# Kernel tuning notes

Hardware: AMD Instinct MI355X
Metric: run time of the kernel (lower is better)

## Reference

```python
import jax, jax.numpy as jnp
import numpy as np

# Qwen3-0.6B-like config; 4 equal-length requests flattened into [R*S, H]
L, R, S, H = 2, 4, 1024, 1024
NH, NKV, DH = 16, 8, 128
FF = 3072
EPS = 1e-6
THETA = 1e6
SCALE = 0.02  # weight init scale to keep activations sane


def setup_inputs() -> dict:
    key = jax.random.key(0)
    ks = jax.random.split(key, 8)
    return {
        "hidden_states": jax.random.normal(ks[0], (R * S, H), jnp.float32),
        "Wq": jax.random.normal(ks[1], (L, H, NH * DH), jnp.float32) * SCALE,
        "Wk": jax.random.normal(ks[2], (L, H, NKV * DH), jnp.float32) * SCALE,
        "Wv": jax.random.normal(ks[3], (L, H, NKV * DH), jnp.float32) * SCALE,
        "Wo": jax.random.normal(ks[4], (L, NH * DH, H), jnp.float32) * SCALE,
        "q_norm_w": jnp.ones((L, DH), jnp.float32),
        "k_norm_w": jnp.ones((L, DH), jnp.float32),
        "ln1_w": jnp.ones((L, H), jnp.float32),
        "ln2_w": jnp.ones((L, H), jnp.float32),
        "Wg": jax.random.normal(ks[5], (L, H, FF), jnp.float32) * SCALE,
        "Wu": jax.random.normal(ks[6], (L, H, FF), jnp.float32) * SCALE,
        "Wd": jax.random.normal(ks[7], (L, FF, H), jnp.float32) * SCALE,
        "final_norm_w": jnp.ones((H,), jnp.float32),
    }


def _rms(x, w):
    return x * jax.lax.rsqrt(jnp.mean(x * x, axis=-1, keepdims=True) + EPS) * w


def _rope_tables():
    inv_freq = 1.0 / (THETA ** (jnp.arange(0, DH, 2, dtype=jnp.float32) / DH))
    pos = jnp.arange(S, dtype=jnp.float32)  # per-request positions 0..S-1 (prefill)
    freqs = pos[:, None] * inv_freq[None, :]        # [S, DH/2]
    emb = jnp.concatenate([freqs, freqs], axis=-1)  # [S, DH]
    return jnp.cos(emb), jnp.sin(emb)


def _rotate_half(x):
    x1, x2 = jnp.split(x, 2, axis=-1)
    return jnp.concatenate([-x2, x1], axis=-1)


def _apply_rope(x, cos, sin):
    # x: [R, heads, S, DH]; cos/sin: [S, DH]
    c = cos[None, None]
    s = sin[None, None]
    return x * c + _rotate_half(x) * s


def reference(hidden_states, Wq, Wk, Wv, Wo, q_norm_w, k_norm_w, ln1_w, ln2_w,
              Wg, Wu, Wd, final_norm_w):
    cos, sin = _rope_tables()
    causal = jnp.tril(jnp.ones((S, S), dtype=bool))  # per-request causal mask
    neg = jnp.finfo(hidden_states.dtype).min
    scaling = 1.0 / jnp.sqrt(jnp.asarray(DH, hidden_states.dtype))

    x = hidden_states
    for l in range(L):
        # --- attention block ---
        residual = x
        h = _rms(x, ln1_w[l])                       # [R*S, H]
        q = (h @ Wq[l]).reshape(R, S, NH, DH)
        k = (h @ Wk[l]).reshape(R, S, NKV, DH)
        v = (h @ Wv[l]).reshape(R, S, NKV, DH)
        q = _rms(q, q_norm_w[l]).transpose(0, 2, 1, 3)   # [R, NH, S, DH]
        k = _rms(k, k_norm_w[l]).transpose(0, 2, 1, 3)   # [R, NKV, S, DH]
        v = v.transpose(0, 2, 1, 3)                      # [R, NKV, S, DH]
        q = _apply_rope(q, cos, sin)
        k = _apply_rope(k, cos, sin)
        # GQA: repeat KV heads
        rep = NH // NKV
        k = jnp.repeat(k, rep, axis=1)
        v = jnp.repeat(v, rep, axis=1)
        scores = jnp.einsum('rhqd,rhkd->rhqk', q, k) * scaling
        scores = jnp.where(causal[None, None], scores, neg)
        attn = jax.nn.softmax(scores, axis=-1)
        o = jnp.einsum('rhqk,rhkd->rhqd', attn, v)       # [R, NH, S, DH]
        o = o.transpose(0, 2, 1, 3).reshape(R * S, NH * DH)
        x = residual + o @ Wo[l]
        # --- MLP block ---
        residual = x
        h = _rms(x, ln2_w[l])
        x = residual + (jax.nn.silu(h @ Wg[l]) * (h @ Wu[l])) @ Wd[l]
    return _rms(x, final_norm_w)
```

## Files before the change

kernel.cpp:

```cpp
#include <hip/hip_runtime.h>
#include <hip/hip_bf16.h>

typedef __bf16 bf16;
typedef __bf16 bf16x8 __attribute__((ext_vector_type(8)));
typedef float f32x4 __attribute__((ext_vector_type(4)));

#define DEVINL __device__ __forceinline__

constexpr int L_ = 2, R_ = 4, S_ = 1024, H_ = 1024;
constexpr int NH_ = 16, NKV_ = 8, DH_ = 128;
constexpr int FF_ = 3072;
constexpr int T_ = R_ * S_;

DEVINL void gload16(const bf16* g, bf16* l) {
    __builtin_amdgcn_global_load_lds(
        (const __attribute__((address_space(1))) void*)g,
        (__attribute__((address_space(3))) void*)l, 16, 0, 0);
}

__global__ void rope_tables_kernel(float* __restrict__ cosb, float* __restrict__ sinb) {
    int s = blockIdx.x;
    int i = threadIdx.x;
    float inv = __expf(-(float)i * (1.0f / 64.0f) * 13.815510557964274f);
    float f = (float)s * inv;
    cosb[s * 64 + i] = cosf(f);
    sinb[s * 64 + i] = sinf(f);
}

template <bool OUT_BF16>
__global__ __launch_bounds__(256) void rmsnorm_kernel(const float* __restrict__ x,
                                                      const float* __restrict__ w,
                                                      void* __restrict__ out) {
    int row = blockIdx.x;
    const float* xr = x + (size_t)row * H_;
    int t = threadIdx.x;
    f32x4 v = *(const f32x4*)(xr + t * 4);
    float ss = v[0] * v[0] + v[1] * v[1] + v[2] * v[2] + v[3] * v[3];
#pragma unroll
    for (int off = 32; off; off >>= 1) ss += __shfl_xor(ss, off);
    __shared__ float part[4];
    if ((t & 63) == 0) part[t >> 6] = ss;
    __syncthreads();
    ss = part[0] + part[1] + part[2] + part[3];
    float r = rsqrtf(ss * (1.0f / (float)H_) + 1e-6f);
    f32x4 wv = *(const f32x4*)(w + t * 4);
#pragma unroll
    for (int j = 0; j < 4; ++j) {
        float o = v[j] * r * wv[j];
        if constexpr (OUT_BF16)
            ((bf16*)out)[(size_t)row * H_ + t * 4 + j] = (bf16)o;
        else
            ((float*)out)[(size_t)row * H_ + t * 4 + j] = o;
    }
}

__global__ __launch_bounds__(256) void transpose_all_kernel(
    const float* __restrict__ Wq, const float* __restrict__ Wk, const float* __restrict__ Wv,
    const float* __restrict__ Wo, const float* __restrict__ Wg, const float* __restrict__ Wu,
    const float* __restrict__ Wd, bf16* __restrict__ wqkv_t, bf16* __restrict__ wo_t,
    bf16* __restrict__ wgu_t, bf16* __restrict__ wd_t) {
    __shared__ float tile[32][33];
    int bid = blockIdx.x;
    const float* in;
    bf16* out;
    int Rk, Cn, mode, tid;
    if (bid < 2048) { in = Wq; out = wqkv_t; Rk = 1024; Cn = 2048; mode = 0; tid = bid; }
    else if (bid < 3072) { in = Wk; out = wqkv_t + (size_t)2048 * 1024; Rk = 1024; Cn = 1024; mode = 0; tid = bid - 2048; }
    else if (bid < 4096) { in = Wv; out = wqkv_t + (size_t)3072 * 1024; Rk = 1024; Cn = 1024; mode = 0; tid = bid - 3072; }
    else if (bid < 6144) { in = Wo; out = wo_t; Rk = 2048; Cn = 1024; mode = 0; tid = bid - 4096; }
    else if (bid < 9216) { in = Wg; out = wgu_t; Rk = 1024; Cn = 3072; mode = 1; tid = bid - 6144; }
    else if (bid < 12288) { in = Wu; out = wgu_t; Rk = 1024; Cn = 3072; mode = 2; tid = bid - 9216; }
    else { in = Wd; out = wd_t; Rk = 3072; Cn = 1024; mode = 0; tid = bid - 12288; }
    int nbx = Cn >> 5;
    int c0 = (tid % nbx) * 32, r0 = (tid / nbx) * 32;
    int t = threadIdx.x;
    int tc = t & 31, tr = t >> 5;
#pragma unroll
    for (int i = 0; i < 4; ++i) {
        int r = tr + i * 8;
        tile[r][tc] = in[(size_t)(r0 + r) * Cn + c0 + tc];
    }
    __syncthreads();
#pragma unroll
    for (int i = 0; i < 4; ++i) {
        int c = c0 + tr + i * 8;
        int n = (mode == 0) ? c : (((c >> 4) << 5) + ((mode == 2) ? 16 : 0) + (c & 15));
        out[(size_t)n * Rk + r0 + tc] = (bf16)tile[tc][tr + i * 8];
    }
}

__global__ __launch_bounds__(256) void vt_kernel(const bf16* __restrict__ qkv,
                                                 bf16* __restrict__ vt) {
    __shared__ bf16 tile[32][34];
    int s0 = blockIdx.x * 32, c0 = blockIdx.y * 32, r = blockIdx.z;
    int t = threadIdx.x, tc = t & 31, tr = t >> 5;
#pragma unroll
    for (int i = 0; i < 4; ++i) {
        int s = tr + i * 8;
        tile[s][tc] = qkv[(size_t)(r * 1024 + s0 + s) * 4096 + 3072 + c0 + tc];
    }
    __syncthreads();
#pragma unroll
    for (int i = 0; i < 4; ++i) {
        int c = tr + i * 8;
        vt[((size_t)(r * 1024 + c0 + c)) * 1024 + s0 + tc] = tile[tc][c];
    }
}

template <int EPI>
__global__ __launch_bounds__(512, 2) void gemmT_kernel(const bf16* __restrict__ A,
                                                       const bf16* __restrict__ Bt,
                                                       void* __restrict__ out,
                                                       int M, int N, int K) {
    __shared__ bf16 lds[49152];
    const int NT = K >> 5;
    int nbm = M >> 8, nbn = N >> 8;
    int slice = nbn >> 3;
    int id = blockIdx.x;
    int xcd = id & 7, wi = id >> 3;
    int bm = (wi / slice) << 8;
    int bn = (xcd * slice + wi % slice) << 8;
    int t = threadIdx.x, lane = t & 63, w = t >> 6;
    int wm = w >> 2, wn = w & 3;
    int hi = lane >> 4, f = lane & 15;

    int r0 = t >> 2;
    int so = (((t & 3) ^ ((r0 >> 1) & 3)) << 3);
    const bf16* aS0 = A + (size_t)(bm + r0) * K + so;
    const bf16* aS1 = A + (size_t)(bm + 128 + r0) * K + so;
    const bf16* bS0 = Bt + (size_t)(bn + r0) * K + so;
    const bf16* bS1 = Bt + (size_t)(bn + 128 + r0) * K + so;

    f32x4 acc[8][4] = {};

    auto stage = [&](int tt, int sb) {
        gload16(aS0 + tt * 32, lds + sb * 8192 + w * 512);
        gload16(aS1 + tt * 32, lds + sb * 8192 + 4096 + w * 512);
        gload16(bS0 + tt * 32, lds + 24576 + sb * 8192 + w * 512);
        gload16(bS1 + tt * 32, lds + 24576 + sb * 8192 + 4096 + w * 512);
    };

    stage(0, 0);
    stage(1, 1);
    asm volatile("s_waitcnt vmcnt(4)" ::: "memory");
    __builtin_amdgcn_s_barrier();

    int cb = 0;
    for (int tau = 0; tau < NT; ++tau) {
        const bf16* aB = lds + cb * 8192;
        const bf16* bB = lds + 24576 + cb * 8192;
        if (tau + 2 < NT) stage(tau + 2, (cb == 0) ? 2 : cb - 1);
        bf16x8 af[8], bfv[4];
#pragma unroll
        for (int mf = 0; mf < 8; ++mf) {
            int row = wm * 128 + mf * 16 + f;
            af[mf] = *(const bf16x8*)(aB + row * 32 + ((hi ^ ((row >> 1) & 3)) << 3));
        }
#pragma unroll
        for (int nf = 0; nf < 4; ++nf) {
            int row = wn * 64 + nf * 16 + f;
            bfv[nf] = *(const bf16x8*)(bB + row * 32 + ((hi ^ ((row >> 1) & 3)) << 3));
        }
        __builtin_amdgcn_s_setprio(1);
#pragma unroll
        for (int mf = 0; mf < 8; ++mf)
#pragma unroll
            for (int nf = 0; nf < 4; ++nf)
                acc[mf][nf] = __builtin_amdgcn_mfma_f32_16x16x32_bf16(af[mf], bfv[nf],
                                                                      acc[mf][nf], 0, 0, 0);
        __builtin_amdgcn_s_setprio(0);
        if (tau < NT - 2)
            asm volatile("s_waitcnt vmcnt(4)" ::: "memory");
        else
            asm volatile("s_waitcnt vmcnt(0)" ::: "memory");
        __builtin_amdgcn_s_barrier();
        cb = (cb == 2) ? 0 : cb + 1;
    }

    int rb = bm + wm * 128 + hi * 4;
    int cb2 = bn + wn * 64 + f;
#pragma unroll
    for (int mf = 0; mf < 8; ++mf)
#pragma unroll
        for (int nf = 0; nf < 4; ++nf)
#pragma unroll
            for (int g = 0; g < 4; ++g)
                ((bf16*)out)[(size_t)(rb + mf * 16 + g) * N + cb2 + nf * 16] =
                    (bf16)acc[mf][nf][g];
}

template <int EPI>
__global__ __launch_bounds__(512, 4) void gemmP_kernel(const bf16* __restrict__ A,
                                                       const bf16* __restrict__ Bt,
                                                       void* __restrict__ out,
                                                       int M, int N, int K) {
    __shared__ bf16 lds[36864];
    const int NT = K >> 5;
    int nbm = M >> 7, nbn = N >> 8;
    int slice = nbn >> 3;
    int id = blockIdx.x;
    int xcd = id & 7, wi = id >> 3;
    int bm = (wi / slice) << 7;
    int bn = (xcd * slice + wi % slice) << 8;
    int t = threadIdx.x, lane = t & 63, w = t >> 6;
    int wm = w >> 2, wn = w & 3;
    int hi = lane >> 4, f = lane & 15;

    int srow = t >> 2;
    int ssc = (t & 3) ^ ((srow >> 1) & 3);
    const bf16* aSrc = A + (size_t)(bm + srow) * K + (ssc << 3);
    const bf16* b0Src = Bt + (size_t)(bn + srow) * K + (ssc << 3);
    const bf16* b1Src = Bt + (size_t)(bn + 128 + srow) * K + (ssc << 3);

    f32x4 acc[4][4] = {};

    auto stage = [&](int tt, int sb) {
        gload16(aSrc + tt * 32, lds + sb * 4096 + w * 512);
        gload16(b0Src + tt * 32, lds + 12288 + sb * 8192 + w * 512);
        gload16(b1Src + tt * 32, lds + 12288 + sb * 8192 + 4096 + w * 512);
    };

    stage(0, 0);
    stage(1, 1);
    asm volatile("s_waitcnt vmcnt(3)" ::: "memory");
    __builtin_amdgcn_s_barrier();

    int cb = 0;
    for (int tau = 0; tau < NT; ++tau) {
        const bf16* aB = lds + cb * 4096;
        const bf16* bB = lds + 12288 + cb * 8192;
        if (tau + 2 < NT) stage(tau + 2, (cb == 0) ? 2 : cb - 1);
        bf16x8 af[4], bfv[4];
#pragma unroll
        for (int mf = 0; mf < 4; ++mf) {
            int row = wm * 64 + mf * 16 + f;
            af[mf] = *(const bf16x8*)(aB + row * 32 + ((hi ^ ((row >> 1) & 3)) << 3));
        }
#pragma unroll
        for (int nf = 0; nf < 4; ++nf) {
            int row = wn * 64 + nf * 16 + f;
            bfv[nf] = *(const bf16x8*)(bB + row * 32 + ((hi ^ ((row >> 1) & 3)) << 3));
        }
        __builtin_amdgcn_s_setprio(1);
#pragma unroll
        for (int mf = 0; mf < 4; ++mf)
#pragma unroll
            for (int nf = 0; nf < 4; ++nf)
                acc[mf][nf] = __builtin_amdgcn_mfma_f32_16x16x32_bf16(af[mf], bfv[nf],
                                                                      acc[mf][nf], 0, 0, 0);
        __builtin_amdgcn_s_setprio(0);
        if (tau < NT - 2)
            asm volatile("s_waitcnt vmcnt(3)" ::: "memory");
        else
            asm volatile("s_waitcnt vmcnt(0)" ::: "memory");
        __builtin_amdgcn_s_barrier();
        cb = (cb == 2) ? 0 : cb + 1;
    }

    int rb = bm + wm * 64 + hi * 4;
#pragma unroll
    for (int mf = 0; mf < 4; ++mf) {
        if constexpr (EPI == 5) {
#pragma unroll
            for (int p = 0; p < 2; ++p) {
                int col = ((bn + wn * 64) >> 1) + p * 16 + f;
#pragma unroll
                for (int g = 0; g < 4; ++g) {
                    float gv = acc[mf][2 * p][g], uv = acc[mf][2 * p + 1][g];
                    float sv = gv / (1.0f + __expf(-gv));
                    ((bf16*)out)[(size_t)(rb + mf * 16 + g) * (N / 2) + col] = (bf16)(sv * uv);
                }
            }
        } else {
            int cb2 = bn + wn * 64 + f;
#pragma unroll
            for (int nf = 0; nf < 4; ++nf)
#pragma unroll
                for (int g = 0; g < 4; ++g)
                    ((bf16*)out)[(size_t)(rb + mf * 16 + g) * N + cb2 + nf * 16] =
                        (bf16)acc[mf][nf][g];
        }
    }
}

template <int EPI>
__global__ __launch_bounds__(256, 2) void gemmD_kernel(const bf16* __restrict__ A,
                                                       const bf16* __restrict__ Bt,
                                                       void* __restrict__ out,
                                                       const float* __restrict__ res,
                                                       int M, int N, int K) {
    __shared__ bf16 lds[36864];
    const int NT = K >> 6;
    int nbm = M >> 6;
    int id = blockIdx.x;
    int xcd = id & 7, wi = id >> 3;
    int bm = (wi % nbm) << 6, bn = xcd << 7;
    int t = threadIdx.x, lane = t & 63, w = t >> 6;
    int wm = w >> 1, wn = w & 1;
    int hi = lane >> 4, f = lane & 15;

    int ar0 = t >> 3, ac0 = t & 7;
    const bf16* aS0 = A + (size_t)(bm + ar0) * K + (((ac0 ^ (ar0 & 7)) & 7) << 3);
    const bf16* aS1 = A + (size_t)(bm + 32 + ar0) * K + (((ac0 ^ ((ar0 + 32) & 7)) & 7) << 3);
    const bf16* bS[4];
#pragma unroll
    for (int j = 0; j < 4; ++j) {
        int row = j * 32 + ar0;
        bS[j] = Bt + (size_t)(bn + row) * K + (((ac0 ^ (row & 7)) & 7) << 3);
    }

    f32x4 acc[2][4] = {};

    auto stage = [&](int tt, int sb) {
        gload16(aS0 + tt * 64, lds + sb * 4096 + w * 512);
        gload16(aS1 + tt * 64, lds + sb * 4096 + 2048 + w * 512);
#pragma unroll
        for (int j = 0; j < 4; ++j)
            gload16(bS[j] + tt * 64, lds + 12288 + sb * 8192 + j * 2048 + w * 512);
    };

    stage(0, 0);
    stage(1, 1);
    asm volatile("s_waitcnt vmcnt(6)" ::: "memory");
    __builtin_amdgcn_s_barrier();

    int cb = 0;
    for (int tau = 0; tau < NT; ++tau) {
        const bf16* aB = lds + cb * 4096;
        const bf16* bB = lds + 12288 + cb * 8192;
        if (tau + 2 < NT) stage(tau + 2, (cb == 0) ? 2 : cb - 1);
        bf16x8 af[2][2], bfv[2][4];
#pragma unroll
        for (int kh = 0; kh < 2; ++kh) {
            int q = kh * 4 + hi;
#pragma unroll
            for (int mf = 0; mf < 2; ++mf) {
                int row = wm * 32 + mf * 16 + f;
                af[kh][mf] = *(const bf16x8*)(aB + row * 64 + ((q ^ (row & 7)) << 3));
            }
#pragma unroll
            for (int nf = 0; nf < 4; ++nf) {
                int row = wn * 64 + nf * 16 + f;
                bfv[kh][nf] = *(const bf16x8*)(bB + row * 64 + ((q ^ (row & 7)) << 3));
            }
        }
        __builtin_amdgcn_s_setprio(1);
#pragma unroll
        for (int kh = 0; kh < 2; ++kh)
#pragma unroll
            for (int mf = 0; mf < 2; ++mf)
#pragma unroll
                for (int nf = 0; nf < 4; ++nf)
                    acc[mf][nf] = __builtin_amdgcn_mfma_f32_16x16x32_bf16(
                        af[kh][mf], bfv[kh][nf], acc[mf][nf], 0, 0, 0);
        __builtin_amdgcn_s_setprio(0);
        if (tau < NT - 2)
            asm volatile("s_waitcnt vmcnt(6)" ::: "memory");
        else
            asm volatile("s_waitcnt vmcnt(0)" ::: "memory");
        __builtin_amdgcn_s_barrier();
        cb = (cb == 2) ? 0 : cb + 1;
    }

    int rb = bm + wm * 32 + hi * 4;
    int cb2 = bn + wn * 64 + f;
#pragma unroll
    for (int mf = 0; mf < 2; ++mf)
#pragma unroll
        for (int nf = 0; nf < 4; ++nf)
#pragma unroll
            for (int g = 0; g < 4; ++g) {
                size_t idx = (size_t)(rb + mf * 16 + g) * N + cb2 + nf * 16;
                ((float*)out)[idx] = acc[mf][nf][g] + res[idx];
            }
}

DEVINL void head_norm_rope(const bf16* __restrict__ src, const float* __restrict__ w,
                           const float* __restrict__ cosb, const float* __restrict__ sinb,
                           int s, int ln, bf16* __restrict__ dst) {
    float x0 = (float)src[ln], x1 = (float)src[ln + 32];
    float x2 = (float)src[ln + 64], x3 = (float)src[ln + 96];
    float ss = x0 * x0 + x1 * x1 + x2 * x2 + x3 * x3;
#pragma unroll
    for (int off = 16; off; off >>= 1) ss += __shfl_xor(ss, off);
    float rr = rsqrtf(ss * (1.0f / 128.0f) + 1e-6f);
    float n0 = x0 * rr * w[ln], n1 = x1 * rr * w[ln + 32];
    float n2 = x2 * rr * w[ln + 64], n3 = x3 * rr * w[ln + 96];
    float c0 = cosb[s * 64 + ln], c1 = cosb[s * 64 + ln + 32];
    float s0 = sinb[s * 64 + ln], s1 = sinb[s * 64 + ln + 32];
    dst[ln] = (bf16)(n0 * c0 - n2 * s0);
    dst[ln + 32] = (bf16)(n1 * c1 - n3 * s1);
    dst[ln + 64] = (bf16)(n2 * c0 + n0 * s0);
    dst[ln + 96] = (bf16)(n3 * c1 + n1 * s1);
}

__global__ __launch_bounds__(256) void qkv_post_kernel(const bf16* __restrict__ qkv,
                                                       const float* __restrict__ qw,
                                                       const float* __restrict__ kw,
                                                       const float* __restrict__ cosb,
                                                       const float* __restrict__ sinb,
                                                       bf16* __restrict__ qo,
                                                       bf16* __restrict__ ko) {
    int tok = blockIdx.x;
    int r = tok >> 10, s = tok & 1023;
    int t = threadIdx.x;
    int g = t >> 5;
    int ln = t & 31;
    const bf16* row = qkv + (size_t)tok * 4096;
#pragma unroll
    for (int hh = 0; hh < 2; ++hh) {
        int h = g + hh * 8;
        head_norm_rope(row + h * 128, qw, cosb, sinb, s, ln,
                       qo + ((size_t)(r * NH_ + h) * S_ + s) * 128);
    }
    head_norm_rope(row + 2048 + g * 128, kw, cosb, sinb, s, ln,
                   ko + ((size_t)(r * NKV_ + g) * S_ + s) * 128);
}

__global__ __launch_bounds__(256, 2) void flash_kernel(const bf16* __restrict__ q,
                                                       const bf16* __restrict__ k,
                                                       const bf16* __restrict__ vt,
                                                       bf16* __restrict__ out) {
    __shared__ bf16 Kl[64 * 128];
    __shared__ bf16 Vl[128 * 64];
    __shared__ bf16 Pl[4][32 * 64];
    int bid = blockIdx.x;
    int grp = bid & 63, slot = bid >> 6;
    int strip = (slot < 4) ? (7 - slot) : (slot - 4);
    int h = 2 * (grp & 7) + ((grp >> 3) & 1);
    int r = grp >> 4;
    int kvh = h >> 1;

    int t = threadIdx.x, lane = t & 63, w = t >> 6;
    int arow = lane & 15, hi = lane >> 4;
    int a7 = arow & 7;
    int grow = hi * 4;
    int qbase = strip * 128 + w * 32;

    const bf16* qp = q + ((size_t)(r * NH_ + h) * S_ + qbase) * 128;
    bf16x8 qf[2][4];
#pragma unroll
    for (int m = 0; m < 2; ++m)
#pragma unroll
        for (int kc = 0; kc < 4; ++kc)
            qf[m][kc] = *(const bf16x8*)(qp + (size_t)(m * 16 + arow) * 128 + kc * 32 + hi * 8);

    const bf16* kp = k + (size_t)(r * NKV_ + kvh) * S_ * 128;
    const bf16* vp = vt + (size_t)(r * NKV_ + kvh) * 128 * S_;

    int krow0 = t >> 4, kc16 = t & 15;
    int vrow0 = t >> 3, vc16 = t & 7;

    bf16x8 ones;
#pragma unroll
    for (int i = 0; i < 8; ++i) ones[i] = (bf16)1.0f;

    f32x4 ao[2][8] = {};
    f32x4 aol[2] = {};
    const float scale = 0.08838834764831845f;

    int nt = 2 * (strip + 1);
    bf16x8 krs[4], vrs[4];
#pragma unroll
    for (int i = 0; i < 4; ++i)
        krs[i] = *(const bf16x8*)(kp + (size_t)(krow0 + 16 * i) * 128 + kc16 * 8);
#pragma unroll
    for (int i = 0; i < 4; ++i)
        vrs[i] = *(const bf16x8*)(vp + (size_t)(vrow0 + 32 * i) * S_ + vc16 * 8);

    for (int it = 0; it < nt; ++it) {
        int kv0 = it * 64;
        __syncthreads();
#pragma unroll
        for (int i = 0; i < 4; ++i) {
            int row = krow0 + 16 * i;
            *(bf16x8*)(&Kl[row * 128 + ((kc16 ^ (row & 7)) * 8)]) = krs[i];
        }
#pragma unroll
        for (int i = 0; i < 4; ++i) {
            int row = vrow0 + 32 * i;
            *(bf16x8*)(&Vl[row * 64 + ((vc16 ^ (row & 7)) * 8)]) = vrs[i];
        }
        __syncthreads();
        if (it + 1 < nt) {
            int kvn = kv0 + 64;
#pragma unroll
            for (int i = 0; i < 4; ++i)
                krs[i] = *(const bf16x8*)(kp + (size_t)(kvn + krow0 + 16 * i) * 128 + kc16 * 8);
#pragma unroll
            for (int i = 0; i < 4; ++i)
                vrs[i] = *(const bf16x8*)(vp + (size_t)(vrow0 + 32 * i) * S_ + kvn + vc16 * 8);
        }
        f32x4 sc[2][4];
#pragma unroll
        for (int m = 0; m < 2; ++m)
#pragma unroll
            for (int n = 0; n < 4; ++n) sc[m][n] = (f32x4){0.f, 0.f, 0.f, 0.f};
#pragma unroll
        for (int n = 0; n < 4; ++n) {
            int krw = n * 16 + arow;
#pragma unroll
            for (int kc = 0; kc < 4; ++kc) {
                bf16x8 kf = *(const bf16x8*)(&Kl[krw * 128 + (((kc * 4 + hi) ^ a7) * 8)]);
                sc[0][n] = __builtin_amdgcn_mfma_f32_16x16x32_bf16(qf[0][kc], kf, sc[0][n], 0, 0, 0);
                sc[1][n] = __builtin_amdgcn_mfma_f32_16x16x32_bf16(qf[1][kc], kf, sc[1][n], 0, 0, 0);
            }
        }
#pragma unroll
        for (int m = 0; m < 2; ++m) {
            bool msk = (kv0 + 64 > qbase + m * 16);
#pragma unroll
            for (int n = 0; n < 4; ++n) {
                int chnk = 2 * n + (arow >> 3);
#pragma unroll
                for (int g = 0; g < 4; ++g) {
                    float sval = sc[m][n][g] * scale;
                    if (msk && (kv0 + n * 16 + arow > qbase + m * 16 + grow + g)) sval = -1e30f;
                    float p = __expf(sval);
                    int qr = m * 16 + grow + g;
                    Pl[w][qr * 64 + ((chnk ^ (qr & 7)) * 8) + a7] = (bf16)p;
                }
            }
        }
        bf16x8 pf[2][2];
#pragma unroll
        for (int m = 0; m < 2; ++m) {
            int qr = m * 16 + arow;
#pragma unroll
            for (int ks = 0; ks < 2; ++ks)
                pf[m][ks] = *(const bf16x8*)(&Pl[w][qr * 64 + (((ks * 4 + hi) ^ a7) * 8)]);
        }
#pragma unroll
        for (int m = 0; m < 2; ++m) {
            aol[m] = __builtin_amdgcn_mfma_f32_16x16x32_bf16(pf[m][0], ones, aol[m], 0, 0, 0);
            aol[m] = __builtin_amdgcn_mfma_f32_16x16x32_bf16(pf[m][1], ones, aol[m], 0, 0, 0);
        }
#pragma unroll
        for (int c = 0; c < 8; ++c) {
            int vrw = c * 16 + arow;
#pragma unroll
            for (int ks = 0; ks < 2; ++ks) {
                bf16x8 vf = *(const bf16x8*)(&Vl[vrw * 64 + (((ks * 4 + hi) ^ a7) * 8)]);
                ao[0][c] = __builtin_amdgcn_mfma_f32_16x16x32_bf16(pf[0][ks], vf, ao[0][c], 0, 0, 0);
                ao[1][c] = __builtin_amdgcn_mfma_f32_16x16x32_bf16(pf[1][ks], vf, ao[1][c], 0, 0, 0);
            }
        }
    }
#pragma unroll
    for (int m = 0; m < 2; ++m) {
        f32x4 rl;
#pragma unroll
        for (int g = 0; g < 4; ++g) rl[g] = 1.0f / aol[m][g];
#pragma unroll
        for (int c = 0; c < 8; ++c)
#pragma unroll
            for (int g = 0; g < 4; ++g) {
                int rq = qbase + m * 16 + grow + g;
                out[(size_t)(r * S_ + rq) * 2048 + h * 128 + c * 16 + arow] =
                    (bf16)(ao[m][c][g] * rl[g]);
            }
    }
}

extern "C" void kernel_launch(void* const* d_in, const int* in_sizes, int n_in,
                              void* d_out, int out_size, void* d_ws, size_t ws_size,
                              hipStream_t stream) {
    const float* hidden = (const float*)d_in[0];
    const float* Wq = (const float*)d_in[1];
    const float* Wk = (const float*)d_in[2];
    const float* Wv = (const float*)d_in[3];
    const float* Wo = (const float*)d_in[4];
    const float* qnw = (const float*)d_in[5];
    const float* knw = (const float*)d_in[6];
    const float* ln1 = (const float*)d_in[7];
    const float* ln2 = (const float*)d_in[8];
    const float* Wg = (const float*)d_in[9];
    const float* Wu = (const float*)d_in[10];
    const float* Wd = (const float*)d_in[11];
    const float* fnw = (const float*)d_in[12];
    float* out = (float*)d_out;

    char* ws = (char*)d_ws;
    size_t off = 0;
    auto alloc = [&](size_t bytes) -> char* {
        char* p = ws + off;
        off += (bytes + 255) & ~(size_t)255;
        return p;
    };
    float* cosb = (float*)alloc((size_t)S_ * 64 * 4);
    float* sinb = (float*)alloc((size_t)S_ * 64 * 4);
    float* x_ws = (float*)alloc((size_t)T_ * H_ * 4);
    bf16* hbuf = (bf16*)alloc((size_t)T_ * H_ * 2);
    bf16* qkv = (bf16*)alloc((size_t)T_ * 4096 * 2);
    bf16* act = qkv;
    bf16* qb = (bf16*)alloc((size_t)R_ * NH_ * S_ * 128 * 2);
    bf16* kb = (bf16*)alloc((size_t)R_ * NKV_ * S_ * 128 * 2);
    bf16* vtb = (bf16*)alloc((size_t)R_ * NKV_ * 128 * S_ * 2);
    bf16* attn = (bf16*)alloc((size_t)T_ * 2048 * 2);
    bf16* wqkv_t = (bf16*)alloc((size_t)4096 * 1024 * 2);
    bf16* wo_t = (bf16*)alloc((size_t)1024 * 2048 * 2);
    bf16* wgu_t = (bf16*)alloc((size_t)6144 * 1024 * 2);
    bf16* wd_t = (bf16*)alloc((size_t)1024 * 3072 * 2);

    rope_tables_kernel<<<S_, 64, 0, stream>>>(cosb, sinb);

    const float* xin = hidden;
    for (int l = 0; l < L_; ++l) {
        transpose_all_kernel<<<15360, 256, 0, stream>>>(
            Wq + (size_t)l * H_ * 2048, Wk + (size_t)l * H_ * 1024, Wv + (size_t)l * H_ * 1024,
            Wo + (size_t)l * 2048 * 1024, Wg + (size_t)l * H_ * 3072, Wu + (size_t)l * H_ * 3072,
            Wd + (size_t)l * 3072 * 1024, wqkv_t, wo_t, wgu_t, wd_t);

        rmsnorm_kernel<true><<<T_, 256, 0, stream>>>(xin, ln1 + (size_t)l * H_, hbuf);
        gemmT_kernel<1><<<256, 512, 0, stream>>>(hbuf, wqkv_t, qkv, 4096, 4096, 1024);
        qkv_post_kernel<<<T_, 256, 0, stream>>>(qkv, qnw + (size_t)l * 128, knw + (size_t)l * 128,
                                                cosb, sinb, qb, kb);
        vt_kernel<<<dim3(32, 32, 4), 256, 0, stream>>>(qkv, vtb);
        flash_kernel<<<512, 256, 0, stream>>>(qb, kb, vtb, attn);
        gemmD_kernel<4><<<512, 256, 0, stream>>>(attn, wo_t, x_ws, xin, 4096, 1024, 2048);
        rmsnorm_kernel<true><<<T_, 256, 0, stream>>>(x_ws, ln2 + (size_t)l * H_, hbuf);
        gemmP_kernel<5><<<768, 512, 0, stream>>>(hbuf, wgu_t, act, 4096, 6144, 1024);
        gemmD_kernel<4><<<512, 256, 0, stream>>>(act, wd_t, x_ws, x_ws, 4096, 1024, 3072);
        xin = x_ws;
    }
    rmsnorm_kernel<false><<<T_, 256, 0, stream>>>(x_ws, fnw, out);
}
```

Baseline: 508.8 us.

## Split K across warp pairs in gemmD with LDS reduction epilogue

The down/output-projection GEMM kernel is reorganized so that the two warp pairs each process alternating 32-wide K slices over the full 64x128 tile, instead of splitting the tile by M. Each warp now holds a 4x4 accumulator block, and the two partial sums are reduced through LDS before the residual-add store. Staging moves to 32-wide K tiles over a 6-slot ring with a new swizzle. The aim is to cut per-warp duplicate LDS fragment reads and raise MFMA work per load, at the cost of more accumulator registers and an extra LDS reduction with two barriers.

```diff
diff --git a/kernel.cpp b/kernel.cpp
--- a/kernel.cpp
+++ b/kernel.cpp
@@ -290,89 +290,102 @@
                                                        const float* __restrict__ res,
                                                        int M, int N, int K) {
     __shared__ bf16 lds[36864];
-    const int NT = K >> 6;
+    const int NP = K >> 6;
     int nbm = M >> 6;
     int id = blockIdx.x;
     int xcd = id & 7, wi = id >> 3;
     int bm = (wi % nbm) << 6, bn = xcd << 7;
     int t = threadIdx.x, lane = t & 63, w = t >> 6;
-    int wm = w >> 1, wn = w & 1;
+    int wn = w & 1, wk = w >> 1;
     int hi = lane >> 4, f = lane & 15;
 
-    int ar0 = t >> 3, ac0 = t & 7;
-    const bf16* aS0 = A + (size_t)(bm + ar0) * K + (((ac0 ^ (ar0 & 7)) & 7) << 3);
-    const bf16* aS1 = A + (size_t)(bm + 32 + ar0) * K + (((ac0 ^ ((ar0 + 32) & 7)) & 7) << 3);
-    const bf16* bS[4];
-#pragma unroll
-    for (int j = 0; j < 4; ++j) {
-        int row = j * 32 + ar0;
-        bS[j] = Bt + (size_t)(bn + row) * K + (((ac0 ^ (row & 7)) & 7) << 3);
-    }
-
-    f32x4 acc[2][4] = {};
-
-    auto stage = [&](int tt, int sb) {
-        gload16(aS0 + tt * 64, lds + sb * 4096 + w * 512);
-        gload16(aS1 + tt * 64, lds + sb * 4096 + 2048 + w * 512);
-#pragma unroll
-        for (int j = 0; j < 4; ++j)
-            gload16(bS[j] + tt * 64, lds + 12288 + sb * 8192 + j * 2048 + w * 512);
+    int r4 = t >> 2, c4 = t & 3;
+    int sw4 = c4 ^ (r4 & 3) ^ ((r4 >> 2) & 3);
+    const bf16* aS = A + (size_t)(bm + r4) * K + sw4 * 8;
+    const bf16* bS0 = Bt + (size_t)(bn + r4) * K + sw4 * 8;
+    const bf16* bS1 = Bt + (size_t)(bn + 64 + r4) * K + sw4 * 8;
+
+    f32x4 acc[4][4] = {};
+
+    auto stageTile = [&](int tt, int st) {
+        gload16(aS + (size_t)tt * 32, lds + st * 6144 + w * 512);
+        gload16(bS0 + (size_t)tt * 32, lds + st * 6144 + 2048 + w * 512);
+        gload16(bS1 + (size_t)tt * 32, lds + st * 6144 + 4096 + w * 512);
     };
 
-    stage(0, 0);
-    stage(1, 1);
+    stageTile(0, 0);
+    stageTile(1, 1);
+    stageTile(2, 2);
+    stageTile(3, 3);
     asm volatile("s_waitcnt vmcnt(6)" ::: "memory");
     __builtin_amdgcn_s_barrier();
 
-    int cb = 0;
-    for (int tau = 0; tau < NT; ++tau) {
-        const bf16* aB = lds + cb * 4096;
-        const bf16* bB = lds + 12288 + cb * 8192;
-        if (tau + 2 < NT) stage(tau + 2, (cb == 0) ? 2 : cb - 1);
-        bf16x8 af[2][2], bfv[2][4];
-#pragma unroll
-        for (int kh = 0; kh < 2; ++kh) {
-            int q = kh * 4 + hi;
-#pragma unroll
-            for (int mf = 0; mf < 2; ++mf) {
-                int row = wm * 32 + mf * 16 + f;
-                af[kh][mf] = *(const bf16x8*)(aB + row * 64 + ((q ^ (row & 7)) << 3));
-            }
-#pragma unroll
-            for (int nf = 0; nf < 4; ++nf) {
-                int row = wn * 64 + nf * 16 + f;
-                bfv[kh][nf] = *(const bf16x8*)(bB + row * 64 + ((q ^ (row & 7)) << 3));
-            }
+    int myslot = wk;
+    int ss = 4;
+    for (int p = 0; p < NP; ++p) {
+        const bf16* aB = lds + myslot * 6144;
+        const bf16* bB = aB + 2048;
+        bool doStage = (p + 2 < NP);
+        if (doStage) {
+            int s1 = (ss == 5) ? 0 : ss + 1;
+            stageTile(2 * p + 4, ss);
+            stageTile(2 * p + 5, s1);
+            ss = (s1 == 5) ? 0 : s1 + 1;
+        }
+        bf16x8 af[4], bfv[4];
+#pragma unroll
+        for (int mf = 0; mf < 4; ++mf) {
+            int row = mf * 16 + f;
+            af[mf] = *(const bf16x8*)(aB + row * 32 +
+                                      ((hi ^ (row & 3) ^ ((row >> 2) & 3)) << 3));
+        }
+#pragma unroll
+        for (int nf = 0; nf < 4; ++nf) {
+            int row = wn * 64 + nf * 16 + f;
+            bfv[nf] = *(const bf16x8*)(bB + row * 32 +
+                                       ((hi ^ (row & 3) ^ ((row >> 2) & 3)) << 3));
         }
         __builtin_amdgcn_s_setprio(1);
 #pragma unroll
-        for (int kh = 0; kh < 2; ++kh)
-#pragma unroll
-            for (int mf = 0; mf < 2; ++mf)
-#pragma unroll
-                for (int nf = 0; nf < 4; ++nf)
-                    acc[mf][nf] = __builtin_amdgcn_mfma_f32_16x16x32_bf16(
-                        af[kh][mf], bfv[kh][nf], acc[mf][nf], 0, 0, 0);
+        for (int mf = 0; mf < 4; ++mf)
+#pragma unroll
+            for (int nf = 0; nf < 4; ++nf)
+                acc[mf][nf] = __builtin_amdgcn_mfma_f32_16x16x32_bf16(af[mf], bfv[nf],
+                                                                      acc[mf][nf], 0, 0, 0);
         __builtin_amdgcn_s_setprio(0);
-        if (tau < NT - 2)
+        if (doStage)
             asm volatile("s_waitcnt vmcnt(6)" ::: "memory");
         else
             asm volatile("s_waitcnt vmcnt(0)" ::: "memory");
         __builtin_amdgcn_s_barrier();
-        cb = (cb == 2) ? 0 : cb + 1;
-    }
-
-    int rb = bm + wm * 32 + hi * 4;
-    int cb2 = bn + wn * 64 + f;
-#pragma unroll
-    for (int mf = 0; mf < 2; ++mf)
-#pragma unroll
-        for (int nf = 0; nf < 4; ++nf)
-#pragma unroll
-            for (int g = 0; g < 4; ++g) {
-                size_t idx = (size_t)(rb + mf * 16 + g) * N + cb2 + nf * 16;
-                ((float*)out)[idx] = acc[mf][nf][g] + res[idx];
+        myslot += 2;
+        if (myslot >= 6) myslot -= 6;
+    }
+
+    __syncthreads();
+    float* fl = (float*)lds;
+    if (wk == 1) {
+#pragma unroll
+        for (int mf = 0; mf < 4; ++mf)
+#pragma unroll
+            for (int nf = 0; nf < 4; ++nf)
+                *(f32x4*)(fl + wn * 4352 + lane * 68 + (mf * 4 + nf) * 4) = acc[mf][nf];
+    }
+    __syncthreads();
+    if (wk == 0) {
+        int cb2 = bn + wn * 64 + f;
+#pragma unroll
+        for (int mf = 0; mf < 4; ++mf)
+#pragma unroll
+            for (int nf = 0; nf < 4; ++nf) {
+                f32x4 o = *(const f32x4*)(fl + wn * 4352 + lane * 68 + (mf * 4 + nf) * 4);
+#pragma unroll
+                for (int g = 0; g < 4; ++g) {
+                    size_t idx = (size_t)(bm + mf * 16 + hi * 4 + g) * N + cb2 + nf * 16;
+                    ((float*)out)[idx] = acc[mf][nf][g] + o[g] + res[idx];
+                }
             }
+    }
 }
 
 DEVINL void head_norm_rope(const bf16* __restrict__ src, const float* __restrict__ w,
```

After: 531.7 us. +4.5%, slower.

## Restructure down-projection GEMM to two waves with 64x64 warp tiles and BK=32

Applied to the files above, without the earlier changes.

The gemmD kernel moves from 4 waves to 2 waves per block, with each wave computing a 64x64 sub-tile (16 accumulators) instead of 32x64. The K step shrinks from 64 to 32 with a matching 4-way LDS swizzle, which halves shared memory per block. The goal is more register-level reuse of fragments per MFMA and more resident blocks from the smaller LDS footprint. In exchange there are fewer waves to hide latency and more loop iterations with barriers.

```diff
diff --git a/kernel.cpp b/kernel.cpp
--- a/kernel.cpp
+++ b/kernel.cpp
@@ -284,39 +284,39 @@
 }
 
 template <int EPI>
-__global__ __launch_bounds__(256, 2) void gemmD_kernel(const bf16* __restrict__ A,
+__global__ __launch_bounds__(128, 2) void gemmD_kernel(const bf16* __restrict__ A,
                                                        const bf16* __restrict__ Bt,
                                                        void* __restrict__ out,
                                                        const float* __restrict__ res,
                                                        int M, int N, int K) {
-    __shared__ bf16 lds[36864];
-    const int NT = K >> 6;
+    __shared__ bf16 lds[18432];
+    const int NT = K >> 5;
     int nbm = M >> 6;
     int id = blockIdx.x;
     int xcd = id & 7, wi = id >> 3;
     int bm = (wi % nbm) << 6, bn = xcd << 7;
     int t = threadIdx.x, lane = t & 63, w = t >> 6;
-    int wm = w >> 1, wn = w & 1;
     int hi = lane >> 4, f = lane & 15;
 
-    int ar0 = t >> 3, ac0 = t & 7;
-    const bf16* aS0 = A + (size_t)(bm + ar0) * K + (((ac0 ^ (ar0 & 7)) & 7) << 3);
-    const bf16* aS1 = A + (size_t)(bm + 32 + ar0) * K + (((ac0 ^ ((ar0 + 32) & 7)) & 7) << 3);
-    const bf16* bS[4];
-#pragma unroll
-    for (int j = 0; j < 4; ++j) {
-        int row = j * 32 + ar0;
-        bS[j] = Bt + (size_t)(bn + row) * K + (((ac0 ^ (row & 7)) & 7) << 3);
-    }
-
-    f32x4 acc[2][4] = {};
+    int r0 = t >> 2;
+    int sw = ((t & 3) ^ ((r0 >> 1) & 3)) << 3;
+    const bf16* aS0 = A + (size_t)(bm + r0) * K + sw;
+    const bf16* aS1 = A + (size_t)(bm + 32 + r0) * K + sw;
+    const bf16* bS0 = Bt + (size_t)(bn + r0) * K + sw;
+    const bf16* bS1 = Bt + (size_t)(bn + 32 + r0) * K + sw;
+    const bf16* bS2 = Bt + (size_t)(bn + 64 + r0) * K + sw;
+    const bf16* bS3 = Bt + (size_t)(bn + 96 + r0) * K + sw;
+
+    f32x4 acc[4][4] = {};
 
     auto stage = [&](int tt, int sb) {
-        gload16(aS0 + tt * 64, lds + sb * 4096 + w * 512);
-        gload16(aS1 + tt * 64, lds + sb * 4096 + 2048 + w * 512);
-#pragma unroll
-        for (int j = 0; j < 4; ++j)
-            gload16(bS[j] + tt * 64, lds + 12288 + sb * 8192 + j * 2048 + w * 512);
+        bf16* base = lds + sb * 6144;
+        gload16(aS0 + tt * 32, base + w * 512);
+        gload16(aS1 + tt * 32, base + 1024 + w * 512);
+        gload16(bS0 + tt * 32, base + 2048 + w * 512);
+        gload16(bS1 + tt * 32, base + 3072 + w * 512);
+        gload16(bS2 + tt * 32, base + 4096 + w * 512);
+        gload16(bS3 + tt * 32, base + 5120 + w * 512);
     };
 
     stage(0, 0);
@@ -326,33 +326,27 @@
 
     int cb = 0;
     for (int tau = 0; tau < NT; ++tau) {
-        const bf16* aB = lds + cb * 4096;
-        const bf16* bB = lds + 12288 + cb * 8192;
+        const bf16* aB = lds + cb * 6144;
+        const bf16* bB = aB + 2048;
         if (tau + 2 < NT) stage(tau + 2, (cb == 0) ? 2 : cb - 1);
-        bf16x8 af[2][2], bfv[2][4];
-#pragma unroll
-        for (int kh = 0; kh < 2; ++kh) {
-            int q = kh * 4 + hi;
-#pragma unroll
-            for (int mf = 0; mf < 2; ++mf) {
-                int row = wm * 32 + mf * 16 + f;
-                af[kh][mf] = *(const bf16x8*)(aB + row * 64 + ((q ^ (row & 7)) << 3));
-            }
-#pragma unroll
-            for (int nf = 0; nf < 4; ++nf) {
-                int row = wn * 64 + nf * 16 + f;
-                bfv[kh][nf] = *(const bf16x8*)(bB + row * 64 + ((q ^ (row & 7)) << 3));
-            }
+        bf16x8 af[4], bfv[4];
+#pragma unroll
+        for (int mf = 0; mf < 4; ++mf) {
+            int row = mf * 16 + f;
+            af[mf] = *(const bf16x8*)(aB + row * 32 + ((hi ^ ((row >> 1) & 3)) << 3));
+        }
+#pragma unroll
+        for (int nf = 0; nf < 4; ++nf) {
+            int row = w * 64 + nf * 16 + f;
+            bfv[nf] = *(const bf16x8*)(bB + row * 32 + ((hi ^ ((row >> 1) & 3)) << 3));
         }
         __builtin_amdgcn_s_setprio(1);
 #pragma unroll
-        for (int kh = 0; kh < 2; ++kh)
-#pragma unroll
-            for (int mf = 0; mf < 2; ++mf)
-#pragma unroll
-                for (int nf = 0; nf < 4; ++nf)
-                    acc[mf][nf] = __builtin_amdgcn_mfma_f32_16x16x32_bf16(
-                        af[kh][mf], bfv[kh][nf], acc[mf][nf], 0, 0, 0);
+        for (int mf = 0; mf < 4; ++mf)
+#pragma unroll
+            for (int nf = 0; nf < 4; ++nf)
+                acc[mf][nf] = __builtin_amdgcn_mfma_f32_16x16x32_bf16(af[mf], bfv[nf],
+                                                                      acc[mf][nf], 0, 0, 0);
         __builtin_amdgcn_s_setprio(0);
         if (tau < NT - 2)
             asm volatile("s_waitcnt vmcnt(6)" ::: "memory");
@@ -362,10 +356,10 @@
         cb = (cb == 2) ? 0 : cb + 1;
     }
 
-    int rb = bm + wm * 32 + hi * 4;
-    int cb2 = bn + wn * 64 + f;
-#pragma unroll
-    for (int mf = 0; mf < 2; ++mf)
+    int rb = bm + hi * 4;
+    int cb2 = bn + w * 64 + f;
+#pragma unroll
+    for (int mf = 0; mf < 4; ++mf)
 #pragma unroll
         for (int nf = 0; nf < 4; ++nf)
 #pragma unroll
@@ -617,10 +611,10 @@
                                                 cosb, sinb, qb, kb);
         vt_kernel<<<dim3(32, 32, 4), 256, 0, stream>>>(qkv, vtb);
         flash_kernel<<<512, 256, 0, stream>>>(qb, kb, vtb, attn);
-        gemmD_kernel<4><<<512, 256, 0, stream>>>(attn, wo_t, x_ws, xin, 4096, 1024, 2048);
+        gemmD_kernel<4><<<512, 128, 0, stream>>>(attn, wo_t, x_ws, xin, 4096, 1024, 2048);
         rmsnorm_kernel<true><<<T_, 256, 0, stream>>>(x_ws, ln2 + (size_t)l * H_, hbuf);
         gemmP_kernel<5><<<768, 512, 0, stream>>>(hbuf, wgu_t, act, 4096, 6144, 1024);
-        gemmD_kernel<4><<<512, 256, 0, stream>>>(act, wd_t, x_ws, x_ws, 4096, 1024, 3072);
+        gemmD_kernel<4><<<512, 128, 0, stream>>>(act, wd_t, x_ws, x_ws, 4096, 1024, 3072);
         xin = x_ws;
     }
     rmsnorm_kernel<false><<<T_, 256, 0, stream>>>(x_ws, fnw, out);
```

Result: slower. 546.7 us (+7.5%).
